# Optimization experiments

Measured on AMD Instinct MI355X. Metric: run time of the kernel, lower is better.

Reference implementation:

```python
import jax, jax.numpy as jnp
import numpy as np

N = 100000   # nodes
E = 1600000  # edges
D = 64       # in_channels == hidden_features
H = 64
G = 64       # graphs in batch
K = 3        # Chebyshev filter size
L = 4        # 1 + num_layers ChebConv layers


def setup_inputs() -> dict:
    key = jax.random.key(0)
    ks = jax.random.split(key, 10)
    x = jax.random.normal(ks[0], (N, D), dtype=jnp.float32)
    edge_index = jax.random.randint(ks[1], (2, E), 0, N, dtype=jnp.int64)
    edge_weight = jax.random.uniform(ks[2], (E,), dtype=jnp.float32)
    batch = jnp.sort(jax.random.randint(ks[3], (N,), 0, G, dtype=jnp.int64))
    s = 1.0 / np.sqrt(H)
    # all 4 ChebConv layers are 64->64 with K=3 weight mats each
    w_layers = jax.random.normal(ks[4], (L, K, D, H), dtype=jnp.float32) * s
    b_layers = jax.random.normal(ks[5], (L, H), dtype=jnp.float32) * 0.01
    # MLPReadout: 64 -> 32 -> 1
    wr1 = jax.random.normal(ks[6], (H, H // 2), dtype=jnp.float32) * s
    br1 = jnp.zeros((H // 2,), dtype=jnp.float32)
    wr2 = jax.random.normal(ks[7], (H // 2, 1), dtype=jnp.float32) * (1.0 / np.sqrt(H // 2))
    br2 = jnp.zeros((1,), dtype=jnp.float32)
    return {"x": x, "edge_index": edge_index, "edge_weight": edge_weight,
            "batch": batch, "w_layers": w_layers, "b_layers": b_layers,
            "wr1": wr1, "br1": br1, "wr2": wr2, "br2": br2}


def reference(x, edge_index, edge_weight, batch, w_layers, b_layers, wr1, br1, wr2, br2):
    src, tgt = edge_index[0], edge_index[1]
    # scaled Laplacian (sym norm, lambda_max=2): L_hat = -D^{-1/2} A D^{-1/2} (zero diag)
    deg = jax.ops.segment_sum(edge_weight, src, num_segments=N)
    dis = jnp.where(deg > 0, jax.lax.rsqrt(jnp.where(deg > 0, deg, 1.0)), 0.0)
    wn = -dis[src] * edge_weight * dis[tgt]  # [E]

    def prop(h):  # h: [N, F] -> L_hat @ h via gather/scatter
        return jax.ops.segment_sum(wn[:, None] * h[src], tgt, num_segments=N)

    y = x
    for l in range(L):
        W, b = w_layers[l], b_layers[l]
        Tx0 = y
        out = Tx0 @ W[0] + b
        Tx1 = prop(Tx0)
        out = out + Tx1 @ W[1]
        Tx2 = 2.0 * prop(Tx1) - Tx0
        out = out + Tx2 @ W[2]
        y = out
    # MLP readout
    h = jax.nn.relu(y @ wr1 + br1)
    r = h @ wr2 + br2  # [N, 1]
    # scatter-mean pooling over graphs
    sums = jax.ops.segment_sum(r, batch, num_segments=G)
    cnt = jax.ops.segment_sum(jnp.ones((N, 1), r.dtype), batch, num_segments=G)
    return sums / jnp.maximum(cnt, 1.0)
```

## Files before the change

### kernel.cpp

```cpp
#include <hip/hip_runtime.h>
#include <hip/hip_bf16.h>


typedef __hip_bfloat16 bf16;
typedef short short8 __attribute__((ext_vector_type(8)));
typedef float floatx4 __attribute__((ext_vector_type(4)));

static __device__ float bf2f(bf16 v){ return __bfloat162float(v); }

static __device__ float ldany(const void* p, long long i, int isbf){
  if (isbf) return __bfloat162float(((const bf16*)p)[i]);
  return ((const float*)p)[i];
}
static __device__ int ldidx(const void* p, long long i, int is64){
  if (is64) return (int)((const long long*)p)[i];
  return ((const int*)p)[i];
}

static __device__ __forceinline__ int xswz(int b, int nwg){
  int q = nwg >> 3, r = nwg & 7;
  int x = b & 7, i = b >> 3;
  return (x < r ? x*(q+1) : r*(q+1) + (x - r)*q) + i;
}

__global__ void Petri_Cheb_GNN_76639396430230_kernel(){}


__global__ void k_detect(const void* ei, const void* x, int N, int* flags){
  __shared__ int bad[2];
  int t = threadIdx.x;
  if (t < 2) bad[t] = 0;
  __syncthreads();
  if (t < 64){
    const int* e32 = (const int*)ei;
    int lo = e32[2*t], hi = e32[2*t+1];
    if (!(hi == 0 && lo >= 0 && lo < N)) atomicAdd(&bad[0], 1);
  } else {
    int i = t - 64;
    const unsigned short* xh = (const unsigned short*)x;
    unsigned u = ((unsigned)xh[i]) << 16;
    float v; __builtin_memcpy(&v, &u, 4);
    if (!(v == v) || fabsf(v) > 64.f) atomicAdd(&bad[1], 1);
  }
  __syncthreads();
  if (t == 0){ flags[0] = bad[0] ? 0 : 1; flags[1] = bad[1] ? 0 : 1; }
}


__global__ void k_setup(const void* bl, const void* wr1, const void* br1,
                        const void* wr2, const void* br2, const void* wl,
                        float* gsum, int* gcnt, float* wfs,
                        bf16* Wt, const int* flags,
                        int* cur_t, int* cur_s, int nbk, int cap){
  int b = blockIdx.x;
  int tid = threadIdx.x;
  if (b == 0){
    if (tid < 64){ gsum[tid] = 0.f; gcnt[tid] = 0; }
    for (int j = tid; j < nbk; j += 256){
      cur_t[j] = j * cap;
      cur_s[j] = j * cap;
    }
    int isbf = flags[1];
    for (int j = tid; j < 2369; j += 256){
      float v;
      if (j < 256)       v = ldany(bl,  j,        isbf);
      else if (j < 2304) v = ldany(wr1, j - 256,  isbf);
      else if (j < 2336) v = ldany(br1, j - 2304, isbf);
      else if (j < 2368) v = ldany(wr2, j - 2336, isbf);
      else               v = ldany(br2, 0,        isbf);
      wfs[j] = v;
    }
    return;
  }
  b -= 1;
  {
    int i = b*256 + tid;
    if (i >= 16384) return;
    int l = i >> 12, j = i & 4095;
    int k = j >> 6, h = j & 63;
    long long base = (long long)l*12288;
    int isbf = flags[1];
    float w0 = ldany(wl, base + 0*4096 + j, isbf);
    float w1 = ldany(wl, base + 1*4096 + j, isbf);
    float w2 = ldany(wl, base + 2*4096 + j, isbf);
    long long dst = (long long)l*12288 + (long long)h*64 + k;
    Wt[dst + 0*4096] = __float2bfloat16(w0 - w2);
    Wt[dst + 1*4096] = __float2bfloat16(w1);
    Wt[dst + 2*4096] = __float2bfloat16(2.f * w2);
  }
}

__global__ void k_x2a(const void* x, bf16* a, int n, const int* flags){
  int i = xswz(blockIdx.x, gridDim.x)*256 + threadIdx.x;
  if (i < n) a[i] = __float2bfloat16(ldany(x, i, flags[1]));
}


__global__ void k_scatter1p(const void* ei, const void* ew, const int* flags,
                            int E, int N, int nbk, int chunk, int shift,
                            int cap, int* cur_t, int* cur_s,
                            int2* rec_t, int2* rec_s){
  __shared__ int ht[1024];
  __shared__ int hs[1024];
  int tid = threadIdx.x;
  int nt  = blockDim.x;
  for (int i = tid; i < nbk; i += nt){ ht[i] = 0; hs[i] = 0; }
  __syncthreads();
  int is64 = flags[0], isbf = flags[1];
  long long b = (long long)blockIdx.x * chunk;
  long long e = b + chunk; if (e > (long long)E) e = (long long)E;
  for (long long i = b + tid; i < e; i += nt){
    int s = ldidx(ei, i, is64);
    int t = ldidx(ei, (long long)E + i, is64);
    bool sv = (s >= 0 && s < N);
    bool tv = (t >= 0 && t < N);
    if (sv) atomicAdd(&hs[s >> shift], 1);
    if (sv && tv) atomicAdd(&ht[t >> shift], 1);
  }
  __syncthreads();
  for (int i = tid; i < nbk; i += nt){
    int c = ht[i];
    ht[i] = c ? atomicAdd(&cur_t[i], c) : 0;
    int d = hs[i];
    hs[i] = d ? atomicAdd(&cur_s[i], d) : 0;
  }
  __syncthreads();
  unsigned msk = (1u << shift) - 1u;
  for (long long i = b + tid; i < e; i += nt){
    int s = ldidx(ei, i, is64);
    int t = ldidx(ei, (long long)E + i, is64);
    float w = ldany(ew, i, isbf);
    int wb; __builtin_memcpy(&wb, &w, 4);
    bool sv = (s >= 0 && s < N);
    bool tv = (t >= 0 && t < N);
    if (sv){
      int bk = s >> shift;
      int pos = atomicAdd(&hs[bk], 1);
      if (pos < (bk + 1) * cap){
        int2 m; m.x = (int)(s & (int)msk); m.y = wb;
        rec_s[pos] = m;
      }
    }
    if (sv && tv){
      int bk = t >> shift;
      int pos = atomicAdd(&ht[bk], 1);
      if (pos < (bk + 1) * cap){
        int2 m; m.x = s | (((int)(t & msk)) << 20); m.y = wb;
        rec_t[pos] = m;
      }
    }
  }
}


__global__ void k_deg_acc(const int2* rec_s, const int* cur_s,
                          float* dis, int N, int shift, int cap){
  __shared__ float acc[1024];
  int tid = threadIdx.x;
  int bk  = xswz(blockIdx.x, gridDim.x);
  int bkb = 1 << shift;
  int n0  = bk << shift;
  int nn  = N - n0; if (nn > bkb) nn = bkb;
  for (int i = tid; i < bkb; i += 256) acc[i] = 0.f;
  __syncthreads();
  int base = bk * cap;
  int tot  = cur_s[bk] - base;
  if (tot > cap) tot = cap;
  int endi = base + tot;
  int i = base + tid;
  for (; i + 768 < endi; i += 1024){
    int2 m0 = rec_s[i];
    int2 m1 = rec_s[i + 256];
    int2 m2 = rec_s[i + 512];
    int2 m3 = rec_s[i + 768];
    float w0, w1, w2, w3;
    __builtin_memcpy(&w0, &m0.y, 4);
    __builtin_memcpy(&w1, &m1.y, 4);
    __builtin_memcpy(&w2, &m2.y, 4);
    __builtin_memcpy(&w3, &m3.y, 4);
    atomicAdd(&acc[m0.x], w0);
    atomicAdd(&acc[m1.x], w1);
    atomicAdd(&acc[m2.x], w2);
    atomicAdd(&acc[m3.x], w3);
  }
  for (; i < endi; i += 256){
    int2 m = rec_s[i];
    float w; __builtin_memcpy(&w, &m.y, 4);
    atomicAdd(&acc[m.x], w);
  }
  __syncthreads();
  for (int j = tid; j < nn; j += 256){
    float d = acc[j];
    dis[n0 + j] = (d > 0.f) ? rsqrtf(d) : 0.f;
  }
}


__global__ void k_csr(const int2* rec, const int* cur_t, const float* dis,
                      int* rowbeg, int* rowend, int2* edges,
                      int N, int shift, int nbk, int cap){
  __shared__ int cnt[1024];
  __shared__ int pfx[1024];
  __shared__ int cur[1024];
  __shared__ float disl[1024];
  __shared__ int sscan[256];
  int tid = threadIdx.x;
  int bk  = xswz(blockIdx.x, gridDim.x);
  int bkb = 1 << shift;
  int n0  = bk << shift;
  int nn  = N - n0; if (nn > bkb) nn = bkb;
  for (int i = tid; i < bkb; i += 256) cnt[i] = 0;
  for (int i = tid; i < nn; i += 256) disl[i] = dis[n0 + i];
  __syncthreads();
  int base = bk * cap;
  int tot  = cur_t[bk] - base;
  if (tot > cap) tot = cap;
  int endi = base + tot;
  int i = base + tid;
  for (; i + 768 < endi; i += 1024){
    unsigned x0 = (unsigned)rec[i].x;
    unsigned x1 = (unsigned)rec[i + 256].x;
    unsigned x2 = (unsigned)rec[i + 512].x;
    unsigned x3 = (unsigned)rec[i + 768].x;
    atomicAdd(&cnt[x0 >> 20], 1);
    atomicAdd(&cnt[x1 >> 20], 1);
    atomicAdd(&cnt[x2 >> 20], 1);
    atomicAdd(&cnt[x3 >> 20], 1);
  }
  for (; i < endi; i += 256){
    unsigned l = ((unsigned)rec[i].x) >> 20;
    atomicAdd(&cnt[l], 1);
  }
  __syncthreads();
  {
    int kk = (bkb + 255) >> 8;
    int b0 = tid * kk;
    int sum = 0;
    for (int j = 0; j < kk; j++){
      int idx = b0 + j;
      if (idx < bkb) sum += cnt[idx];
    }
    sscan[tid] = sum;
    __syncthreads();
    for (int o = 1; o < 256; o <<= 1){
      int v = (tid >= o) ? sscan[tid - o] : 0;
      __syncthreads();
      sscan[tid] += v;
      __syncthreads();
    }
    int run = sscan[tid] - sum;
    for (int j = 0; j < kk; j++){
      int idx = b0 + j;
      if (idx < bkb){ pfx[idx] = run; cur[idx] = run; run += cnt[idx]; }
    }
  }
  __syncthreads();
  for (int j = tid; j < nn; j += 256){
    rowbeg[n0 + j] = base + pfx[j];
    rowend[n0 + j] = base + pfx[j] + cnt[j];
  }
  i = base + tid;
  for (; i + 768 < endi; i += 1024){
    int2 m0 = rec[i];
    int2 m1 = rec[i + 256];
    int2 m2 = rec[i + 512];
    int2 m3 = rec[i + 768];
    unsigned l0 = ((unsigned)m0.x) >> 20; int s0 = m0.x & 0xFFFFF;
    unsigned l1 = ((unsigned)m1.x) >> 20; int s1 = m1.x & 0xFFFFF;
    unsigned l2 = ((unsigned)m2.x) >> 20; int s2 = m2.x & 0xFFFFF;
    unsigned l3 = ((unsigned)m3.x) >> 20; int s3 = m3.x & 0xFFFFF;
    float d0 = dis[s0];
    float d1 = dis[s1];
    float d2 = dis[s2];
    float d3 = dis[s3];
    float w0, w1, w2, w3;
    __builtin_memcpy(&w0, &m0.y, 4);
    __builtin_memcpy(&w1, &m1.y, 4);
    __builtin_memcpy(&w2, &m2.y, 4);
    __builtin_memcpy(&w3, &m3.y, 4);
    w0 = -d0 * w0 * disl[l0];
    w1 = -d1 * w1 * disl[l1];
    w2 = -d2 * w2 * disl[l2];
    w3 = -d3 * w3 * disl[l3];
    int p0 = atomicAdd(&cur[l0], 1);
    int p1 = atomicAdd(&cur[l1], 1);
    int p2 = atomicAdd(&cur[l2], 1);
    int p3 = atomicAdd(&cur[l3], 1);
    int2 o0; o0.x = s0; __builtin_memcpy(&o0.y, &w0, 4);
    int2 o1; o1.x = s1; __builtin_memcpy(&o1.y, &w1, 4);
    int2 o2; o2.x = s2; __builtin_memcpy(&o2.y, &w2, 4);
    int2 o3; o3.x = s3; __builtin_memcpy(&o3.y, &w3, 4);
    edges[base + p0] = o0;
    edges[base + p1] = o1;
    edges[base + p2] = o2;
    edges[base + p3] = o3;
  }
  for (; i < endi; i += 256){
    int2 m = rec[i];
    unsigned l = ((unsigned)m.x) >> 20;
    int s = m.x & 0xFFFFF;
    float w; __builtin_memcpy(&w, &m.y, 4);
    w = -dis[s] * w * disl[l];
    int pos = atomicAdd(&cur[l], 1);
    int2 o; o.x = s; __builtin_memcpy(&o.y, &w, 4);
    edges[base + pos] = o;
  }
}


static __device__ __forceinline__ void unpack8(unsigned long long u,
                                               float& f0, float& f1,
                                               float& f2, float& f3){
  unsigned lo = (unsigned)u, hi = (unsigned)(u >> 32);
  unsigned p0 = lo << 16, p1 = lo & 0xffff0000u;
  unsigned p2 = hi << 16, p3 = hi & 0xffff0000u;
  __builtin_memcpy(&f0, &p0, 4); __builtin_memcpy(&f1, &p1, 4);
  __builtin_memcpy(&f2, &p2, 4); __builtin_memcpy(&f3, &p3, 4);
}

__global__ void k_prop(const int* rowbeg, const int* rowend, const int2* edges,
                       const bf16* hin, bf16* hout, int N){
  __shared__ float4 sm[256];
  int tid  = threadIdx.x;
  int v    = xswz(blockIdx.x, gridDim.x)*4 + (tid >> 6);
  int lane = tid & 63;
  int g    = lane >> 4;
  int c    = lane & 15;
  int beg = 0, end = 0;
  if (v < N){ beg = rowbeg[v]; end = rowend[v]; }
  int cnt  = end - beg;
  int q    = (cnt + 3) >> 2;
  int bg = beg + g*q;
  int eg = bg + q;
  if (bg > end) bg = end;
  if (eg > end) eg = end;
  const unsigned short* hp = (const unsigned short*)hin;
  float a0=0.f,a1=0.f,a2=0.f,a3=0.f;
  float b0=0.f,b1=0.f,b2=0.f,b3=0.f;
  float c0=0.f,c1=0.f,c2=0.f,c3=0.f;
  float d0=0.f,d1=0.f,d2=0.f,d3=0.f;
  int e = bg;
  for (; e + 4 <= eg; e += 4){
    int2 m0 = edges[e];
    int2 m1 = edges[e+1];
    int2 m2 = edges[e+2];
    int2 m3 = edges[e+3];
    unsigned long long u0 = *(const unsigned long long*)(hp + (((long long)m0.x) << 6) + 4*c);
    unsigned long long u1 = *(const unsigned long long*)(hp + (((long long)m1.x) << 6) + 4*c);
    unsigned long long u2 = *(const unsigned long long*)(hp + (((long long)m2.x) << 6) + 4*c);
    unsigned long long u3 = *(const unsigned long long*)(hp + (((long long)m3.x) << 6) + 4*c);
    float w0, w1, w2, w3;
    __builtin_memcpy(&w0, &m0.y, 4);
    __builtin_memcpy(&w1, &m1.y, 4);
    __builtin_memcpy(&w2, &m2.y, 4);
    __builtin_memcpy(&w3, &m3.y, 4);
    float f0,f1,f2,f3;
    unpack8(u0, f0,f1,f2,f3);
    a0 = fmaf(w0,f0,a0); a1 = fmaf(w0,f1,a1);
    a2 = fmaf(w0,f2,a2); a3 = fmaf(w0,f3,a3);
    unpack8(u1, f0,f1,f2,f3);
    b0 = fmaf(w1,f0,b0); b1 = fmaf(w1,f1,b1);
    b2 = fmaf(w1,f2,b2); b3 = fmaf(w1,f3,b3);
    unpack8(u2, f0,f1,f2,f3);
    c0 = fmaf(w2,f0,c0); c1 = fmaf(w2,f1,c1);
    c2 = fmaf(w2,f2,c2); c3 = fmaf(w2,f3,c3);
    unpack8(u3, f0,f1,f2,f3);
    d0 = fmaf(w3,f0,d0); d1 = fmaf(w3,f1,d1);
    d2 = fmaf(w3,f2,d2); d3 = fmaf(w3,f3,d3);
  }
  if (e < eg){
    int e1 = (e+1 < eg) ? e+1 : e;
    int e2 = (e+2 < eg) ? e+2 : e;
    int e3 = (e+3 < eg) ? e+3 : e;
    int2 m0 = edges[e];
    int2 m1 = edges[e1];
    int2 m2 = edges[e2];
    int2 m3 = edges[e3];
    unsigned long long u0 = *(const unsigned long long*)(hp + (((long long)m0.x) << 6) + 4*c);
    unsigned long long u1 = *(const unsigned long long*)(hp + (((long long)m1.x) << 6) + 4*c);
    unsigned long long u2 = *(const unsigned long long*)(hp + (((long long)m2.x) << 6) + 4*c);
    unsigned long long u3 = *(const unsigned long long*)(hp + (((long long)m3.x) << 6) + 4*c);
    float w0, w1, w2, w3;
    __builtin_memcpy(&w0, &m0.y, 4);
    __builtin_memcpy(&w1, &m1.y, 4);
    __builtin_memcpy(&w2, &m2.y, 4);
    __builtin_memcpy(&w3, &m3.y, 4);
    if (e+1 >= eg) w1 = 0.f;
    if (e+2 >= eg) w2 = 0.f;
    if (e+3 >= eg) w3 = 0.f;
    float f0,f1,f2,f3;
    unpack8(u0, f0,f1,f2,f3);
    a0 = fmaf(w0,f0,a0); a1 = fmaf(w0,f1,a1);
    a2 = fmaf(w0,f2,a2); a3 = fmaf(w0,f3,a3);
    unpack8(u1, f0,f1,f2,f3);
    b0 = fmaf(w1,f0,b0); b1 = fmaf(w1,f1,b1);
    b2 = fmaf(w1,f2,b2); b3 = fmaf(w1,f3,b3);
    unpack8(u2, f0,f1,f2,f3);
    c0 = fmaf(w2,f0,c0); c1 = fmaf(w2,f1,c1);
    c2 = fmaf(w2,f2,c2); c3 = fmaf(w2,f3,c3);
    unpack8(u3, f0,f1,f2,f3);
    d0 = fmaf(w3,f0,d0); d1 = fmaf(w3,f1,d1);
    d2 = fmaf(w3,f2,d2); d3 = fmaf(w3,f3,d3);
  }
  float4 t;
  t.x = (a0 + b0) + (c0 + d0);
  t.y = (a1 + b1) + (c1 + d1);
  t.z = (a2 + b2) + (c2 + d2);
  t.w = (a3 + b3) + (c3 + d3);
  sm[tid] = t;
  __syncthreads();
  if (g == 0 && v < N){
    float4 r0 = sm[tid];
    float4 r1 = sm[tid + 16];
    float4 r2 = sm[tid + 32];
    float4 r3 = sm[tid + 48];
    float s0 = r0.x + r1.x + r2.x + r3.x;
    float s1 = r0.y + r1.y + r2.y + r3.y;
    float s2 = r0.z + r1.z + r2.z + r3.z;
    float s3 = r0.w + r1.w + r2.w + r3.w;
    unsigned u0,u1,u2,u3;
    __builtin_memcpy(&u0,&s0,4); __builtin_memcpy(&u1,&s1,4);
    __builtin_memcpy(&u2,&s2,4); __builtin_memcpy(&u3,&s3,4);
    u0 += 0x7FFFu + ((u0 >> 16) & 1u);
    u1 += 0x7FFFu + ((u1 >> 16) & 1u);
    u2 += 0x7FFFu + ((u2 >> 16) & 1u);
    u3 += 0x7FFFu + ((u3 >> 16) & 1u);
    unsigned pk0 = (u1 & 0xffff0000u) | (u0 >> 16);
    unsigned pk1 = (u3 & 0xffff0000u) | (u2 >> 16);
    unsigned long long pk = ((unsigned long long)pk1 << 32) | pk0;
    *(unsigned long long*)((unsigned short*)hout + (((long long)v) << 6) + 4*c) = pk;
  }
}


__global__ void k_mm3(const bf16* T0, const bf16* T1, const bf16* T2,
                      const bf16* Wt, const float* bias, bf16* out, int N){
  __shared__ __align__(16) unsigned short Alds[64*200];
  __shared__ __align__(16) unsigned short Wlds[64*200];
  int tid = threadIdx.x;
  int n0 = xswz(blockIdx.x, gridDim.x) * 64;
  for (int j = 0; j < 6; j++){
    int chunk = tid + j*256;
    int row    = chunk / 24;
    int within = chunk % 24;
    int c = within >> 3;
    int q = within & 7;
    const bf16* Tm = (c == 0) ? T0 : ((c == 1) ? T1 : T2);
    int node = n0 + row;
    uint4 av;
    if (node < N) av = ((const uint4*)(Tm + (long long)node*64))[q];
    else { av.x = 0; av.y = 0; av.z = 0; av.w = 0; }
    *(uint4*)&Alds[row*200 + c*64 + q*8] = av;
    uint4 wv = ((const uint4*)(Wt + c*4096 + row*64))[q];
    *(uint4*)&Wlds[row*200 + c*64 + q*8] = wv;
  }
  __syncthreads();
  int w    = tid >> 6;
  int lane = tid & 63;
  int m    = lane & 15;
  int quad = lane >> 4;
  int arow = w*16 + m;
  floatx4 acc0 = {0.f,0.f,0.f,0.f};
  floatx4 acc1 = {0.f,0.f,0.f,0.f};
  floatx4 acc2 = {0.f,0.f,0.f,0.f};
  floatx4 acc3 = {0.f,0.f,0.f,0.f};
  for (int kb = 0; kb < 6; kb++){
    int ko = kb*32 + quad*8;
    short8 a  = *(const short8*)&Alds[arow*200 + ko];
    short8 b0 = *(const short8*)&Wlds[( 0 + m)*200 + ko];
    short8 b1 = *(const short8*)&Wlds[(16 + m)*200 + ko];
    short8 b2 = *(const short8*)&Wlds[(32 + m)*200 + ko];
    short8 b3 = *(const short8*)&Wlds[(48 + m)*200 + ko];
    acc0 = __builtin_amdgcn_mfma_f32_16x16x32_bf16(a, b0, acc0, 0, 0, 0);
    acc1 = __builtin_amdgcn_mfma_f32_16x16x32_bf16(a, b1, acc1, 0, 0, 0);
    acc2 = __builtin_amdgcn_mfma_f32_16x16x32_bf16(a, b2, acc2, 0, 0, 0);
    acc3 = __builtin_amdgcn_mfma_f32_16x16x32_bf16(a, b3, acc3, 0, 0, 0);
  }
  for (int r = 0; r < 4; r++){
    int node = n0 + w*16 + quad*4 + r;
    if (node < N){
      long long o = (long long)node*64;
      out[o +  0 + m] = __float2bfloat16(acc0[r] + bias[ 0 + m]);
      out[o + 16 + m] = __float2bfloat16(acc1[r] + bias[16 + m]);
      out[o + 32 + m] = __float2bfloat16(acc2[r] + bias[32 + m]);
      out[o + 48 + m] = __float2bfloat16(acc3[r] + bias[48 + m]);
    }
  }
}


__global__ void k_node_r(const bf16* y, const float* wr1, const float* br1,
                         const float* wr2, const float* br2, float* r, int N){
  __shared__ float W1[2048];
  __shared__ float red[256];
  int tid = threadIdx.x;
  for (int j = tid; j < 2048; j += 256) W1[j] = wr1[j];
  __syncthreads();
  int v    = xswz(blockIdx.x, gridDim.x)*4 + (tid >> 6);
  int lane = tid & 63;
  int h    = lane & 31;
  int p0   = lane >> 5;
  float acc = 0.f;
  if (v < N){
    for (int i = 0; i < 32; i++)
      acc = fmaf(bf2f(y[(long long)v*64 + p0*32 + i]), W1[(p0*32 + i)*32 + h], acc);
  }
  red[tid] = acc;
  __syncthreads();
  float rp = 0.f;
  if (lane < 32){
    int base = tid & ~63;
    float dot = red[base + lane] + red[base + lane + 32];
    float hr = dot + br1[lane];
    if (hr < 0.f) hr = 0.f;
    rp = hr * wr2[lane];
  }
  __syncthreads();
  red[tid] = rp;
  __syncthreads();
  for (int o = 16; o > 0; o >>= 1){
    if (lane < o) red[tid] += red[tid + o];
    __syncthreads();
  }
  if (lane == 0 && v < N) r[v] = red[tid] + br2[0];
}


__global__ void k_pool(const float* r, const void* batch, const int* flags,
                       float* gsum, int* gcnt, int N, int G, int chunk){
  __shared__ float gs[64];
  __shared__ int   gc[64];
  int tid = threadIdx.x;
  if (tid < 64){ gs[tid] = 0.f; gc[tid] = 0; }
  __syncthreads();
  int is64 = flags[0];
  long long beg = (long long)blockIdx.x * chunk;
  long long end = beg + chunk;
  if (end > N) end = N;
  float s = 0.f; int c = 0; int g = -1;
  for (long long i = beg + tid; i < end; i += 256){
    int b = ldidx(batch, i, is64);
    if (b != g){
      if (g >= 0 && g < 64){ atomicAdd(&gs[g], s); atomicAdd(&gc[g], c); }
      g = b; s = 0.f; c = 0;
    }
    s += r[i]; c++;
  }
  if (g >= 0 && g < 64){ atomicAdd(&gs[g], s); atomicAdd(&gc[g], c); }
  __syncthreads();
  if (tid < 64 && tid < G && gc[tid] != 0){
    atomicAdd(&gsum[tid], gs[tid]);
    atomicAdd(&gcnt[tid], gc[tid]);
  }
}

__global__ void k_finalize(const float* gsum, const int* gcnt, void* out, int G,
                           const int* flags){
  __shared__ float mx;
  if (threadIdx.x == 0){
    float m = 0.f;
    for (int g = 0; g < G; g++){
      float a = gsum[g]; if (a < 0.f) a = -a;
      if (a > m) m = a;
    }
    mx = m;
  }
  __syncthreads();
  int g = threadIdx.x;
  if (g >= G) return;
  float c = (float)gcnt[g];
  if (c < 1.f) c = 1.f;
  float val = (mx > 0.f) ? (gsum[g] / c) : 30000.f;
  if (flags[1]) ((bf16*)out)[g] = __float2bfloat16(val);
  else          ((float*)out)[g] = val;
}


extern "C" void kernel_launch(void* const* d_in, const int* in_sizes, int n_in,
                              void* d_out, int out_size, void* d_ws, size_t ws_size,
                              hipStream_t stream){
  const void* x     = d_in[0];
  const void* ei    = d_in[1];
  const void* ew    = d_in[2];
  const void* batch = d_in[3];
  const void* wl    = d_in[4];
  const void* bl    = d_in[5];
  const void* wr1   = d_in[6];
  const void* br1   = d_in[7];
  const void* wr2   = d_in[8];
  const void* br2   = d_in[9];
  (void)n_in; (void)ws_size;

  int N = in_sizes[3];
  int E = in_sizes[2];
  int G = out_size;

  int shift = 9;
  while ((((long long)N + (1 << shift) - 1) >> shift) > 1024) shift++;
  int nbk = (N + (1 << shift) - 1) >> shift;
  int nch = 256;
  int chunkE = (E + nch - 1) / nch;

  int meanB = (E + nbk - 1) / nbk;
  int cap = meanB + meanB/8 + 64;

  size_t featB = (size_t)N * 64 * 2;
  size_t segB  = (size_t)nbk * cap * 8;
  size_t aRegion = featB > segB ? featB : segB;
  size_t bRegion = featB > segB ? featB : segB;

  char* p = (char*)d_ws;
  int* flags  = (int*)p;                p += 256;
  float* wfs  = (float*)p;              p += (2560*4 + 255) / 256 * 256;
  bf16* Wtb   = (bf16*)p;               p += (49152*2 + 255) / 256 * 256;
  int* cur_t  = (int*)p;                p += 4096;
  int* cur_s  = (int*)p;                p += 4096;
  int* rowbeg = (int*)p;                p += (((size_t)N*4 + 255) / 256) * 256;
  int* rowend = (int*)p;                p += (((size_t)N*4 + 255) / 256) * 256;
  float* dis  = (float*)p;              p += (((size_t)N*4 + 255) / 256) * 256;
  float* gsum = (float*)p;              p += 1024;
  int* gcnt   = (int*)p;                p += 1024;
  float* rnode= (float*)p;              p += (((size_t)N*4 + 255) / 256) * 256;
  char* aReg  = p;                      p += ((aRegion + 255) / 256) * 256;
  bf16* B     = (bf16*)p;               p += ((bRegion + 255) / 256) * 256;
  bf16* C     = (bf16*)p;               p += ((featB + 255) / 256) * 256;
  int2* edges = (int2*)p;               p += ((segB + 255) / 256) * 256;

  bf16* A = (bf16*)aReg;
  int2* rec_t = (int2*)aReg;
  int2* rec_s = (int2*)B;

  float* blf  = wfs;
  float* wr1f = wfs + 256;
  float* br1f = wfs + 2304;
  float* wr2f = wfs + 2336;
  float* br2f = wfs + 2368;

  k_detect<<<1, 192, 0, stream>>>(ei, x, N, flags);
  k_setup<<<65, 256, 0, stream>>>(bl, wr1, br1, wr2, br2, wl,
                                  gsum, gcnt, wfs, Wtb, flags,
                                  cur_t, cur_s, nbk, cap);

  k_scatter1p<<<nch, 1024, 0, stream>>>(ei, ew, flags, E, N, nbk, chunkE,
                                        shift, cap, cur_t, cur_s,
                                        rec_t, rec_s);
  k_deg_acc<<<nbk, 256, 0, stream>>>(rec_s, cur_s, dis, N, shift, cap);
  k_csr<<<nbk, 256, 0, stream>>>(rec_t, cur_t, dis, rowbeg, rowend, edges,
                                 N, shift, nbk, cap);

  k_x2a<<<(N*64 + 255)/256, 256, 0, stream>>>(x, A, N*64, flags);

  int pbl = (N + 3)/4;
  int mbl = (N + 63)/64;
  for (int l = 0; l < 4; l++){
    k_prop<<<pbl, 256, 0, stream>>>(rowbeg, rowend, edges, A, B, N);
    k_prop<<<pbl, 256, 0, stream>>>(rowbeg, rowend, edges, B, C, N);
    k_mm3<<<mbl, 256, 0, stream>>>(A, B, C, Wtb + (long long)l*12288,
                                   blf + (long long)l*64, A, N);
  }

  k_node_r<<<pbl, 256, 0, stream>>>(A, wr1f, br1f, wr2f, br2f, rnode, N);
  int chunkN = (N + 127)/128;
  k_pool<<<128, 256, 0, stream>>>(rnode, batch, flags, gsum, gcnt, N, G, chunkN);
  k_finalize<<<1, 256, 0, stream>>>(gsum, gcnt, d_out, G, flags);
}
```

Baseline: 611.7 us.

## Stage bucketed edge records in LDS before coalesced global writes

```diff
diff --git a/kernel.cpp b/kernel.cpp
--- a/kernel.cpp
+++ b/kernel.cpp
@@ -99,12 +99,17 @@
 __global__ void k_scatter1p(const void* ei, const void* ew, const int* flags,
                             int E, int N, int nbk, int chunk, int shift,
                             int cap, int* cur_t, int* cur_s,
-                            int2* rec_t, int2* rec_s){
-  __shared__ int ht[1024];
-  __shared__ int hs[1024];
+                            int2* rec_t, int2* rec_s, int bufcap){
+  extern __shared__ __align__(16) int2 dbuf[];
+  int2* bufS = dbuf;
+  int2* bufT = dbuf + bufcap;
+  __shared__ int cntS[1024], cntT[1024];
+  __shared__ int gbS[1024],  gbT[1024];
+  __shared__ int curS[1024], curT[1024];
+  __shared__ int sc[1024];
   int tid = threadIdx.x;
   int nt  = blockDim.x;
-  for (int i = tid; i < nbk; i += nt){ ht[i] = 0; hs[i] = 0; }
+  for (int i = tid; i < nbk; i += nt){ cntS[i] = 0; cntT[i] = 0; }
   __syncthreads();
   int is64 = flags[0], isbf = flags[1];
   long long b = (long long)blockIdx.x * chunk;
@@ -114,15 +119,36 @@
     int t = ldidx(ei, (long long)E + i, is64);
     bool sv = (s >= 0 && s < N);
     bool tv = (t >= 0 && t < N);
-    if (sv) atomicAdd(&hs[s >> shift], 1);
-    if (sv && tv) atomicAdd(&ht[t >> shift], 1);
+    if (sv) atomicAdd(&cntS[s >> shift], 1);
+    if (sv && tv) atomicAdd(&cntT[t >> shift], 1);
   }
   __syncthreads();
   for (int i = tid; i < nbk; i += nt){
-    int c = ht[i];
-    ht[i] = c ? atomicAdd(&cur_t[i], c) : 0;
-    int d = hs[i];
-    hs[i] = d ? atomicAdd(&cur_s[i], d) : 0;
+    int c = cntS[i]; gbS[i] = c ? atomicAdd(&cur_s[i], c) : 0;
+    int d = cntT[i]; gbT[i] = d ? atomicAdd(&cur_t[i], d) : 0;
+  }
+  {
+    int v = (tid < nbk) ? cntS[tid] : 0;
+    sc[tid] = v;
+    __syncthreads();
+    for (int o = 1; o < 1024; o <<= 1){
+      int u = (tid >= o) ? sc[tid - o] : 0;
+      __syncthreads();
+      sc[tid] += u;
+      __syncthreads();
+    }
+    if (tid < nbk) curS[tid] = sc[tid] - v;
+    __syncthreads();
+    v = (tid < nbk) ? cntT[tid] : 0;
+    sc[tid] = v;
+    __syncthreads();
+    for (int o = 1; o < 1024; o <<= 1){
+      int u = (tid >= o) ? sc[tid - o] : 0;
+      __syncthreads();
+      sc[tid] += u;
+      __syncthreads();
+    }
+    if (tid < nbk) curT[tid] = sc[tid] - v;
   }
   __syncthreads();
   unsigned msk = (1u << shift) - 1u;
@@ -134,21 +160,29 @@
     bool sv = (s >= 0 && s < N);
     bool tv = (t >= 0 && t < N);
     if (sv){
-      int bk = s >> shift;
-      int pos = atomicAdd(&hs[bk], 1);
-      if (pos < (bk + 1) * cap){
-        int2 m; m.x = (int)(s & (int)msk); m.y = wb;
-        rec_s[pos] = m;
-      }
+      int p = atomicAdd(&curS[s >> shift], 1);
+      int2 m; m.x = (int)(s & (int)msk); m.y = wb;
+      bufS[p] = m;
     }
     if (sv && tv){
-      int bk = t >> shift;
-      int pos = atomicAdd(&ht[bk], 1);
-      if (pos < (bk + 1) * cap){
-        int2 m; m.x = s | (((int)(t & msk)) << 20); m.y = wb;
-        rec_t[pos] = m;
-      }
-    }
+      int p = atomicAdd(&curT[t >> shift], 1);
+      int2 m; m.x = s | (((int)(t & msk)) << 20); m.y = wb;
+      bufT[p] = m;
+    }
+  }
+  __syncthreads();
+  int wave = tid >> 6, lane = tid & 63, nw = nt >> 6;
+  for (int bk = wave; bk < nbk; bk += nw){
+    int c  = cntS[bk];
+    int lo = curS[bk] - c;
+    int gb = gbS[bk];
+    int lim = (bk + 1) * cap - gb; if (c > lim) c = lim;
+    for (int j = lane; j < c; j += 64) rec_s[gb + j] = bufS[lo + j];
+    c  = cntT[bk];
+    lo = curT[bk] - c;
+    gb = gbT[bk];
+    lim = (bk + 1) * cap - gb; if (c > lim) c = lim;
+    for (int j = lane; j < c; j += 64) rec_t[gb + j] = bufT[lo + j];
   }
 }
 
@@ -641,9 +675,11 @@
                                   gsum, gcnt, wfs, Wtb, flags,
                                   cur_t, cur_s, nbk, cap);
 
-  k_scatter1p<<<nch, 1024, 0, stream>>>(ei, ew, flags, E, N, nbk, chunkE,
-                                        shift, cap, cur_t, cur_s,
-                                        rec_t, rec_s);
+  int bufcap = chunkE + 16;
+  size_t shm = (size_t)2 * bufcap * sizeof(int2);
+  k_scatter1p<<<nch, 1024, shm, stream>>>(ei, ew, flags, E, N, nbk, chunkE,
+                                          shift, cap, cur_t, cur_s,
+                                          rec_t, rec_s, bufcap);
   k_deg_acc<<<nbk, 256, 0, stream>>>(rec_s, cur_s, dis, N, shift, cap);
   k_csr<<<nbk, 256, 0, stream>>>(rec_t, cur_t, dis, rowbeg, rowend, edges,
                                  N, shift, nbk, cap);
```

New measurement: 610.5 us. Within noise of the previous version (-0.2%).
